# Kernel optimization log

Hardware: AMD Instinct MI355X
Metric: run time of the kernel (lower is better)

Reference implementation:

```python
import jax, jax.numpy as jnp
import numpy as np

POOL_H, POOL_W = 16, 8
NEG = -1e30
B, C = 8, 64
F_WR2 = 64 * 32 * 32          # flattened x3
D_CLS = 3 * C * POOL_H * POOL_W  # 24576, classifier input


def _adaptive_mask(starts, lens, out_size, in_size):
    """Membership mask (B, out_size, in_size) for torch-style adaptive pooling bins
    over a per-sample window [start, start+len) along an axis of length in_size."""
    i = jnp.arange(out_size)
    lo = (i[None, :] * lens[:, None]) // out_size                     # (B,O)
    hi = ((i[None, :] + 1) * lens[:, None] + out_size - 1) // out_size  # ceil
    r = jnp.arange(in_size)
    rel = r[None, None, :] - starts[:, None, None]                    # (B,1,I)
    return (rel >= lo[:, :, None]) & (rel < hi[:, :, None]) & (rel >= 0) & (rel < lens[:, None, None])


def _roi_pool(x, boxes):
    """Adaptive max pool of per-sample ROI boxes (x1,y1,x2,y2) to (16,8).
    x: (B,C,H,W,T); invalid boxes -> zeros (matches torch code's skip/zeros fallback)."""
    _, _, H, W, T = x.shape
    b = jnp.floor(boxes).astype(jnp.int32)          # torch .long() after clamp>=0
    x1, y1, x2, y2 = b[:, 0], b[:, 1], b[:, 2], b[:, 3]
    valid = (x1 >= 0) & (y1 >= 0) & (x2 < W) & (y2 < H) & (x2 > x1) & (y2 > y1)
    h = jnp.maximum(y2 - y1 + 1, 1)                 # inclusive slice y1:y2+1
    w = jnp.maximum(x2 - x1 + 1, 1)
    rowm = _adaptive_mask(y1, h, POOL_H, H)         # (B,16,H)
    colm = _adaptive_mask(x1, w, POOL_W, W)         # (B,8,W)
    # separable masked max: first over W into 8 col-bins, then over H into 16 row-bins
    s1 = jnp.max(jnp.where(colm[:, None, None, :, :, None], x[:, :, :, None, :, :], NEG), axis=4)  # (B,C,H,8,T)
    s2 = jnp.max(jnp.where(rowm[:, None, :, :, None, None], s1[:, :, None, :, :, :], NEG), axis=(3, 5))  # (B,C,16,8)
    ok = valid[:, None, None, None] & (s2 > NEG / 2)
    return jnp.where(ok, s2, 0.0)


def _forward(x1, x2, x3,
             wr2_w1, wr2_b1, wr2_w2, wr2_b2, wr2_w3, wr2_b3,
             head_w1, head_b1, w2_prov, b2_prov, w2_alpha, b2_alpha, w2_ad, b2_ad):
    bsz = x3.shape[0]
    xf = x3.reshape(bsz, -1)
    # wR2: three stacked Linears, no nonlinearity
    boxLoc = ((xf @ wr2_w1 + wr2_b1) @ wr2_w2 + wr2_b2) @ wr2_w3 + wr2_b3   # (B,4)
    postfix = jnp.array([[1., 0., 1., 0.], [0., 1., 0., 1.],
                         [-0.5, 0., 0.5, 0.], [0., -0.5, 0., 0.5]], dtype=boxLoc.dtype)
    boxNew = jnp.clip(boxLoc @ postfix, 0.0, 1.0)                           # (B,4) in [0,1]

    def scale(x):  # p matrices are diag(w,h,w,h)
        H, W = x.shape[2], x.shape[3]
        return jnp.array([W, H, W, H], dtype=boxNew.dtype)

    roi1 = _roi_pool(x1, boxNew * scale(x1))
    roi2 = _roi_pool(x2, boxNew * scale(x2))
    roi3 = _roi_pool(x3, boxNew * scale(x3))
    feat = jnp.concatenate((roi1, roi2, roi3), axis=1).reshape(bsz, -1)     # (B, 3*C*16*8)

    # 7 classifier heads: Linear(D,128) -> ReLU -> Linear(128, out_k)
    hidden = jax.nn.relu(jnp.einsum('bd,kdh->kbh', feat, head_w1) + head_b1[:, None, :])  # (7,B,128)
    o1 = hidden[0] @ w2_prov + b2_prov          # (B,38)
    o2 = hidden[1] @ w2_alpha + b2_alpha        # (B,25)
    o_ad = jnp.einsum('kbh,kho->kbo', hidden[2:], w2_ad) + b2_ad[:, None, :]  # (5,B,35)
    return (o1, o2, o_ad[0], o_ad[1], o_ad[2], o_ad[3], o_ad[4])


def setup_inputs() -> dict:
    key = jax.random.key(0)
    ks = jax.random.split(key, 16)
    inp = {
        'x1': jax.random.normal(ks[0], (B, C, 128, 128, 1), jnp.float32),
        'x2': jax.random.normal(ks[1], (B, C, 64, 64, 1), jnp.float32),
        'x3': jax.random.normal(ks[2], (B, C, 32, 32, 1), jnp.float32),
        'detection_targets': jax.random.uniform(ks[3], (B, 4), jnp.float32),
        'YI': jax.random.randint(ks[4], (B, 7), 0, 35, jnp.int32),
        # wR2 params (small weights + centered bias so predicted boxes are valid)
        'wr2_w1': jax.random.normal(ks[5], (F_WR2, 100), jnp.float32) * 1e-3,
        'wr2_b1': jnp.zeros((100,), jnp.float32),
        'wr2_w2': jax.random.normal(ks[6], (100, 100), jnp.float32) * 0.05,
        'wr2_b2': jnp.zeros((100,), jnp.float32),
        'wr2_w3': jax.random.normal(ks[7], (100, 4), jnp.float32) * 0.05,
        'wr2_b3': jnp.array([0.5, 0.5, 0.6, 0.6], jnp.float32),
        # 7 heads, first layer stacked
        'head_w1': jax.random.normal(ks[8], (7, D_CLS, 128), jnp.float32) * 0.02,
        'head_b1': jnp.zeros((7, 128), jnp.float32),
        'w2_prov': jax.random.normal(ks[9], (128, 38), jnp.float32) * 0.05,
        'b2_prov': jnp.zeros((38,), jnp.float32),
        'w2_alpha': jax.random.normal(ks[10], (128, 25), jnp.float32) * 0.05,
        'b2_alpha': jnp.zeros((25,), jnp.float32),
        'w2_ad': jax.random.normal(ks[11], (5, 128, 35), jnp.float32) * 0.05,
        'b2_ad': jnp.zeros((5, 35), jnp.float32),
    }
    return inp


def reference(x1, x2, x3, detection_targets, YI,
              wr2_w1, wr2_b1, wr2_w2, wr2_b2, wr2_w3, wr2_b3,
              head_w1, head_b1, w2_prov, b2_prov, w2_alpha, b2_alpha, w2_ad, b2_ad):
    # detection_targets / YI are accepted but unused, as in the torch forward
    del detection_targets, YI
    return _forward(x1, x2, x3, wr2_w1, wr2_b1, wr2_w2, wr2_b2, wr2_w3, wr2_b3,
                    head_w1, head_b1, w2_prov, b2_prov, w2_alpha, b2_alpha, w2_ad, b2_ad)
```

## Files before the change

### kernel.cpp

```cpp
#include <hip/hip_runtime.h>

#define Bb 8
#define Cch 64
#define D1 65536
#define D2 24576
#define NCH1 512
#define CH1 128
#define NCH2 192
#define CH2 128
#define NEGV -1e30f


__global__ __launch_bounds__(128) void k_gemm1(const float* __restrict__ x3,
                                               const float* __restrict__ w1,
                                               float* __restrict__ p1) {
    __shared__ float xs[Bb][CH1];
    int c = blockIdx.x, t = threadIdx.x;
    int d0 = c * CH1;
    #pragma unroll
    for (int b = 0; b < Bb; ++b) xs[b][t] = x3[(size_t)b * D1 + d0 + t];
    __syncthreads();
    if (t < 100) {
        float acc[Bb];
        #pragma unroll
        for (int b = 0; b < Bb; ++b) acc[b] = 0.f;
        #pragma unroll 4
        for (int dl = 0; dl < CH1; ++dl) {
            float w = w1[(size_t)(d0 + dl) * 100 + t];
            #pragma unroll
            for (int b = 0; b < Bb; ++b) acc[b] += w * xs[b][dl];
        }
        #pragma unroll
        for (int b = 0; b < Bb; ++b) p1[((size_t)c * 100 + t) * 8 + b] = acc[b];
    }
}

__global__ __launch_bounds__(64) void k_red1(const float* __restrict__ p1,
                                             const float* __restrict__ b1,
                                             float* __restrict__ h1) {
    int hb = blockIdx.x;
    int h = hb >> 3, b = hb & 7;
    int t = threadIdx.x;
    float s = 0.f;
    #pragma unroll 4
    for (int c = t; c < NCH1; c += 64) s += p1[((size_t)c * 100 + h) * 8 + b];
    for (int off = 32; off; off >>= 1) s += __shfl_down(s, off);
    if (t == 0) h1[b * 100 + h] = s + b1[h];
}

__global__ __launch_bounds__(256) void k_tail(const float* __restrict__ h1g,
                                              const float* __restrict__ w2,
                                              const float* __restrict__ b2,
                                              const float* __restrict__ w3,
                                              const float* __restrict__ b3,
                                              float* __restrict__ boxNew) {
    __shared__ float h1s[800], h2s[800], bl[32];
    int t = threadIdx.x;
    for (int i = t; i < 800; i += 256) h1s[i] = h1g[i];
    __syncthreads();
    for (int i = t; i < 800; i += 256) {
        int b = i / 100, j = i % 100;
        float s = b2[j];
        for (int k = 0; k < 100; ++k) s += h1s[b * 100 + k] * w2[k * 100 + j];
        h2s[i] = s;
    }
    __syncthreads();
    if (t < 32) {
        int b = t >> 2, m = t & 3;
        float s = b3[m];
        for (int j = 0; j < 100; ++j) s += h2s[b * 100 + j] * w3[j * 4 + m];
        bl[t] = s;
    }
    __syncthreads();
    if (t < 32) {
        int b = t >> 2, i = t & 3;
        float l0 = bl[b * 4 + 0], l1 = bl[b * 4 + 1];
        float l2 = bl[b * 4 + 2], l3 = bl[b * 4 + 3];
        float v = (i == 0) ? l0 - 0.5f * l2
                : (i == 1) ? l1 - 0.5f * l3
                : (i == 2) ? l0 + 0.5f * l2
                           : l1 + 0.5f * l3;
        boxNew[t] = fminf(fmaxf(v, 0.f), 1.f);
    }
}

__global__ __launch_bounds__(128) void k_roi(const float* __restrict__ x1,
                                             const float* __restrict__ x2,
                                             const float* __restrict__ x3,
                                             const float* __restrict__ boxNew,
                                             float* __restrict__ feat) {
    int bid = blockIdx.x;
    int s = bid >> 9, r = bid & 511;
    int b = r >> 6, c = r & 63;
    const float* x = (s == 0) ? x1 : (s == 1) ? x2 : x3;
    int H = (s == 0) ? 128 : (s == 1) ? 64 : 32;
    float bn0 = boxNew[b * 4 + 0], bn1 = boxNew[b * 4 + 1];
    float bn2 = boxNew[b * 4 + 2], bn3 = boxNew[b * 4 + 3];
    float Hf = (float)H;
    int ix1 = (int)floorf(bn0 * Hf);
    int iy1 = (int)floorf(bn1 * Hf);
    int ix2 = (int)floorf(bn2 * Hf);
    int iy2 = (int)floorf(bn3 * Hf);
    bool valid = (ix1 >= 0) && (iy1 >= 0) && (ix2 < H) && (iy2 < H) &&
                 (ix2 > ix1) && (iy2 > iy1);
    int t = threadIdx.x;
    float res = 0.f;
    if (valid) {
        int hh = iy2 - iy1 + 1, ww = ix2 - ix1 + 1;
        int ph = t >> 3, pw = t & 7;
        int rlo = (ph * hh) >> 4;
        int rhi = min((((ph + 1) * hh) + 15) >> 4, hh);
        int clo = (pw * ww) >> 3;
        int chi = min((((pw + 1) * ww) + 7) >> 3, ww);
        float m = NEGV;
        const float* base = x + (size_t)(b * Cch + c) * H * H;
        for (int rr = rlo; rr < rhi; ++rr) {
            const float* row = base + (size_t)(iy1 + rr) * H + ix1;
            for (int cc = clo; cc < chi; ++cc) m = fmaxf(m, row[cc]);
        }
        if (m > -5e29f) res = m;
    }
    feat[(size_t)b * D2 + (s * 64 + c) * 128 + t] = res;
}

__global__ __launch_bounds__(256) void k_gemm2(const float* __restrict__ feat,
                                               const float* __restrict__ hw1,
                                               float* __restrict__ p2) {
    __shared__ float fs[Bb][CH2];
    __shared__ float red[128][9];
    int bid = blockIdx.x;
    int k = bid / NCH2, c = bid % NCH2;
    int d0 = c * CH2;
    int t = threadIdx.x;
    for (int i = t; i < Bb * CH2; i += 256) {
        int b = i >> 7, dl = i & 127;
        fs[b][dl] = feat[(size_t)b * D2 + d0 + dl];
    }
    __syncthreads();
    int h = t & 127, dd = t >> 7;
    float acc[Bb];
    #pragma unroll
    for (int b = 0; b < Bb; ++b) acc[b] = 0.f;
    const float* wbase = hw1 + ((size_t)k * D2 + d0) * 128 + h;
    #pragma unroll 8
    for (int dl = dd; dl < CH2; dl += 2) {
        float w = wbase[(size_t)dl * 128];
        #pragma unroll
        for (int b = 0; b < Bb; ++b) acc[b] += w * fs[b][dl];
    }
    if (dd == 1) {
        #pragma unroll
        for (int b = 0; b < Bb; ++b) red[h][b] = acc[b];
    }
    __syncthreads();
    if (dd == 0) {
        #pragma unroll
        for (int b = 0; b < Bb; ++b) {
            float v = acc[b] + red[h][b];
            p2[(((size_t)k * NCH2 + c) * 8 + b) * 128 + h] = v;
        }
    }
}

__global__ __launch_bounds__(128) void k_out(const float* __restrict__ p2,
                                             const float* __restrict__ hb1,
                                             const float* __restrict__ w2p,
                                             const float* __restrict__ b2p,
                                             const float* __restrict__ w2a,
                                             const float* __restrict__ b2a,
                                             const float* __restrict__ w2ad,
                                             const float* __restrict__ b2ad,
                                             float* __restrict__ out) {
    __shared__ float hid[128];
    int kb = blockIdx.x;
    int k = kb >> 3, b = kb & 7;
    int t = threadIdx.x;
    float s = 0.f;
    #pragma unroll 8
    for (int c = 0; c < NCH2; ++c)
        s += p2[(((size_t)k * NCH2 + c) * 8 + b) * 128 + t];
    s += hb1[k * 128 + t];
    hid[t] = fmaxf(s, 0.f);
    __syncthreads();

    const float* w;
    const float* bias;
    int nj, off;
    if (k == 0)      { w = w2p;                    bias = b2p;               nj = 38; off = b * 38; }
    else if (k == 1) { w = w2a;                    bias = b2a;               nj = 25; off = 304 + b * 25; }
    else             { int g = k - 2;
                       w = w2ad + (size_t)g * 128 * 35; bias = b2ad + g * 35; nj = 35;
                       off = 504 + g * 280 + b * 35; }
    if (t < nj) {
        float o = bias[t];
        #pragma unroll 8
        for (int h = 0; h < 128; ++h) o += hid[h] * w[(size_t)h * nj + t];
        out[off + t] = o;
    }
}

extern "C" void kernel_launch(void* const* d_in, const int* in_sizes, int n_in,
                              void* d_out, int out_size, void* d_ws, size_t ws_size,
                              hipStream_t stream) {
    const float* x1   = (const float*)d_in[0];
    const float* x2   = (const float*)d_in[1];
    const float* x3   = (const float*)d_in[2];
    const float* w1   = (const float*)d_in[5];
    const float* b1   = (const float*)d_in[6];
    const float* w2   = (const float*)d_in[7];
    const float* b2   = (const float*)d_in[8];
    const float* w3   = (const float*)d_in[9];
    const float* b3   = (const float*)d_in[10];
    const float* hw1  = (const float*)d_in[11];
    const float* hb1  = (const float*)d_in[12];
    const float* w2p  = (const float*)d_in[13];
    const float* b2p  = (const float*)d_in[14];
    const float* w2a  = (const float*)d_in[15];
    const float* b2a  = (const float*)d_in[16];
    const float* w2ad = (const float*)d_in[17];
    const float* b2ad = (const float*)d_in[18];

    float* ws     = (float*)d_ws;
    float* boxNew = ws;
    float* h1     = ws + 32;
    float* feat   = ws + 8192;
    float* p1     = ws + 204800;
    float* p2     = ws + 614400;

    k_gemm1<<<NCH1, 128, 0, stream>>>(x3, w1, p1);
    k_red1<<<800, 64, 0, stream>>>(p1, b1, h1);
    k_tail<<<1, 256, 0, stream>>>(h1, w2, b2, w3, b3, boxNew);
    k_roi<<<1536, 128, 0, stream>>>(x1, x2, x3, boxNew, feat);
    k_gemm2<<<7 * NCH2, 256, 0, stream>>>(feat, hw1, p2);
    k_out<<<56, 128, 0, stream>>>(p2, hb1, w2p, b2p, w2a, b2a, w2ad, b2ad,
                                  (float*)d_out);
}
```

Baseline: 275.1 us.

## Split reductions across more threads in gemm1, red1, gemm2, out; stage tail weights in LDS

k_gemm1 now uses 256 threads, with two halves each covering 64 rows of the chunk and combining through shared memory. k_red1 uses one block per hidden unit that reduces all 8 batches at once, with coalesced loads. k_gemm2 has each thread load float2 weight pairs over a 4-way split of the chunk. k_out splits its chunk sum over two thread halves, and k_tail stages w2 and w3 in LDS. The aim is more memory parallelism and fewer serial dependent loads, mainly in the weight-streaming GEMMs, at the cost of extra shared-memory reductions and syncs.

Measured after the change: 259.8 us. 1.06x faster.

```diff
diff --git a/kernel.cpp b/kernel.cpp
--- a/kernel.cpp
+++ b/kernel.cpp
@@ -11,41 +11,64 @@
 #define NEGV -1e30f
 
 
-__global__ __launch_bounds__(128) void k_gemm1(const float* __restrict__ x3,
+__global__ __launch_bounds__(256) void k_gemm1(const float* __restrict__ x3,
                                                const float* __restrict__ w1,
                                                float* __restrict__ p1) {
     __shared__ float xs[Bb][CH1];
+    __shared__ float red[CH1][9];
     int c = blockIdx.x, t = threadIdx.x;
     int d0 = c * CH1;
+    for (int i = t; i < Bb * CH1; i += 256) {
+        int b = i >> 7, r = i & 127;
+        xs[b][r] = x3[(size_t)b * D1 + d0 + r];
+    }
+    __syncthreads();
+    int j = t & 127, sub = t >> 7;
+    float acc[Bb];
     #pragma unroll
-    for (int b = 0; b < Bb; ++b) xs[b][t] = x3[(size_t)b * D1 + d0 + t];
-    __syncthreads();
-    if (t < 100) {
-        float acc[Bb];
-        #pragma unroll
-        for (int b = 0; b < Bb; ++b) acc[b] = 0.f;
-        #pragma unroll 4
-        for (int dl = 0; dl < CH1; ++dl) {
-            float w = w1[(size_t)(d0 + dl) * 100 + t];
+    for (int b = 0; b < Bb; ++b) acc[b] = 0.f;
+    if (j < 100) {
+        const float* wb = w1 + (size_t)(d0 + sub * 64) * 100 + j;
+        #pragma unroll 8
+        for (int r0 = 0; r0 < 64; ++r0) {
+            float w = wb[(size_t)r0 * 100];
+            int r = sub * 64 + r0;
             #pragma unroll
-            for (int b = 0; b < Bb; ++b) acc[b] += w * xs[b][dl];
-        }
-        #pragma unroll
-        for (int b = 0; b < Bb; ++b) p1[((size_t)c * 100 + t) * 8 + b] = acc[b];
-    }
-}
-
-__global__ __launch_bounds__(64) void k_red1(const float* __restrict__ p1,
-                                             const float* __restrict__ b1,
-                                             float* __restrict__ h1) {
-    int hb = blockIdx.x;
-    int h = hb >> 3, b = hb & 7;
-    int t = threadIdx.x;
+            for (int b = 0; b < Bb; ++b) acc[b] += w * xs[b][r];
+        }
+    }
+    if (sub == 1 && j < 100) {
+        #pragma unroll
+        for (int b = 0; b < Bb; ++b) red[j][b] = acc[b];
+    }
+    __syncthreads();
+    if (sub == 0 && j < 100) {
+        #pragma unroll
+        for (int b = 0; b < Bb; ++b)
+            p1[((size_t)c * 100 + j) * 8 + b] = acc[b] + red[j][b];
+    }
+}
+
+__global__ __launch_bounds__(256) void k_red1(const float* __restrict__ p1,
+                                              const float* __restrict__ b1,
+                                              float* __restrict__ h1) {
+    __shared__ float red[4][8];
+    int h = blockIdx.x;
+    int t = threadIdx.x;
+    int b = t & 7, c0 = t >> 3;
     float s = 0.f;
-    #pragma unroll 4
-    for (int c = t; c < NCH1; c += 64) s += p1[((size_t)c * 100 + h) * 8 + b];
-    for (int off = 32; off; off >>= 1) s += __shfl_down(s, off);
-    if (t == 0) h1[b * 100 + h] = s + b1[h];
+    #pragma unroll
+    for (int i = 0; i < 16; ++i) {
+        int c = c0 + 32 * i;
+        s += p1[((size_t)c * 100 + h) * 8 + b];
+    }
+    for (int off = 32; off >= 8; off >>= 1) s += __shfl_down(s, off);
+    if ((t & 63) < 8) red[t >> 6][t & 7] = s;
+    __syncthreads();
+    if (t < 8) {
+        float v = red[0][t] + red[1][t] + red[2][t] + red[3][t] + b1[h];
+        h1[t * 100 + h] = v;
+    }
 }
 
 __global__ __launch_bounds__(256) void k_tail(const float* __restrict__ h1g,
@@ -55,20 +78,26 @@
                                               const float* __restrict__ b3,
                                               float* __restrict__ boxNew) {
     __shared__ float h1s[800], h2s[800], bl[32];
-    int t = threadIdx.x;
+    __shared__ float w2s[10000];
+    __shared__ float w3s[400];
+    int t = threadIdx.x;
+    for (int i = t; i < 10000; i += 256) w2s[i] = w2[i];
     for (int i = t; i < 800; i += 256) h1s[i] = h1g[i];
+    for (int i = t; i < 400; i += 256) w3s[i] = w3[i];
     __syncthreads();
     for (int i = t; i < 800; i += 256) {
         int b = i / 100, j = i % 100;
         float s = b2[j];
-        for (int k = 0; k < 100; ++k) s += h1s[b * 100 + k] * w2[k * 100 + j];
+        #pragma unroll 4
+        for (int k = 0; k < 100; ++k) s += h1s[b * 100 + k] * w2s[k * 100 + j];
         h2s[i] = s;
     }
     __syncthreads();
     if (t < 32) {
         int b = t >> 2, m = t & 3;
         float s = b3[m];
-        for (int j = 0; j < 100; ++j) s += h2s[b * 100 + j] * w3[j * 4 + m];
+        #pragma unroll 4
+        for (int j = 0; j < 100; ++j) s += h2s[b * 100 + j] * w3s[j * 4 + m];
         bl[t] = s;
     }
     __syncthreads();
@@ -127,7 +156,7 @@
                                                const float* __restrict__ hw1,
                                                float* __restrict__ p2) {
     __shared__ float fs[Bb][CH2];
-    __shared__ float red[128][9];
+    __shared__ float red[3][64][17];
     int bid = blockIdx.x;
     int k = bid / NCH2, c = bid % NCH2;
     int d0 = c * CH2;
@@ -137,32 +166,43 @@
         fs[b][dl] = feat[(size_t)b * D2 + d0 + dl];
     }
     __syncthreads();
-    int h = t & 127, dd = t >> 7;
-    float acc[Bb];
+    int l = t & 63, sub = t >> 6;
+    int h2 = l * 2;
+    float accx[Bb], accy[Bb];
     #pragma unroll
-    for (int b = 0; b < Bb; ++b) acc[b] = 0.f;
-    const float* wbase = hw1 + ((size_t)k * D2 + d0) * 128 + h;
+    for (int b = 0; b < Bb; ++b) { accx[b] = 0.f; accy[b] = 0.f; }
+    const float* wbase = hw1 + ((size_t)k * D2 + d0) * 128 + h2;
     #pragma unroll 8
-    for (int dl = dd; dl < CH2; dl += 2) {
-        float w = wbase[(size_t)dl * 128];
-        #pragma unroll
-        for (int b = 0; b < Bb; ++b) acc[b] += w * fs[b][dl];
-    }
-    if (dd == 1) {
-        #pragma unroll
-        for (int b = 0; b < Bb; ++b) red[h][b] = acc[b];
-    }
-    __syncthreads();
-    if (dd == 0) {
+    for (int i = 0; i < 32; ++i) {
+        int dl = sub + 4 * i;
+        float2 w = *(const float2*)&wbase[(size_t)dl * 128];
         #pragma unroll
         for (int b = 0; b < Bb; ++b) {
-            float v = acc[b] + red[h][b];
-            p2[(((size_t)k * NCH2 + c) * 8 + b) * 128 + h] = v;
-        }
-    }
-}
-
-__global__ __launch_bounds__(128) void k_out(const float* __restrict__ p2,
+            float f = fs[b][dl];
+            accx[b] += w.x * f;
+            accy[b] += w.y * f;
+        }
+    }
+    if (sub) {
+        #pragma unroll
+        for (int b = 0; b < Bb; ++b) {
+            red[sub - 1][l][b * 2]     = accx[b];
+            red[sub - 1][l][b * 2 + 1] = accy[b];
+        }
+    }
+    __syncthreads();
+    if (sub == 0) {
+        #pragma unroll
+        for (int b = 0; b < Bb; ++b) {
+            float vx = accx[b] + red[0][l][b * 2]     + red[1][l][b * 2]     + red[2][l][b * 2];
+            float vy = accy[b] + red[0][l][b * 2 + 1] + red[1][l][b * 2 + 1] + red[2][l][b * 2 + 1];
+            float2 v = make_float2(vx, vy);
+            *(float2*)&p2[(((size_t)k * NCH2 + c) * 8 + b) * 128 + h2] = v;
+        }
+    }
+}
+
+__global__ __launch_bounds__(256) void k_out(const float* __restrict__ p2,
                                              const float* __restrict__ hb1,
                                              const float* __restrict__ w2p,
                                              const float* __restrict__ b2p,
@@ -172,15 +212,18 @@
                                              const float* __restrict__ b2ad,
                                              float* __restrict__ out) {
     __shared__ float hid[128];
+    __shared__ float red[128];
     int kb = blockIdx.x;
     int k = kb >> 3, b = kb & 7;
     int t = threadIdx.x;
+    int h = t & 127, sub = t >> 7;
     float s = 0.f;
     #pragma unroll 8
-    for (int c = 0; c < NCH2; ++c)
-        s += p2[(((size_t)k * NCH2 + c) * 8 + b) * 128 + t];
-    s += hb1[k * 128 + t];
-    hid[t] = fmaxf(s, 0.f);
+    for (int c = sub; c < NCH2; c += 2)
+        s += p2[(((size_t)k * NCH2 + c) * 8 + b) * 128 + h];
+    if (sub) red[h] = s;
+    __syncthreads();
+    if (!sub) hid[h] = fmaxf(s + red[h] + hb1[k * 128 + h], 0.f);
     __syncthreads();
 
     const float* w;
@@ -194,7 +237,7 @@
     if (t < nj) {
         float o = bias[t];
         #pragma unroll 8
-        for (int h = 0; h < 128; ++h) o += hid[h] * w[(size_t)h * nj + t];
+        for (int hh = 0; hh < 128; ++hh) o += hid[hh] * w[(size_t)hh * nj + t];
         out[off + t] = o;
     }
 }
@@ -227,11 +270,11 @@
     float* p1     = ws + 204800;
     float* p2     = ws + 614400;
 
-    k_gemm1<<<NCH1, 128, 0, stream>>>(x3, w1, p1);
-    k_red1<<<800, 64, 0, stream>>>(p1, b1, h1);
+    k_gemm1<<<NCH1, 256, 0, stream>>>(x3, w1, p1);
+    k_red1<<<100, 256, 0, stream>>>(p1, b1, h1);
     k_tail<<<1, 256, 0, stream>>>(h1, w2, b2, w3, b3, boxNew);
     k_roi<<<1536, 128, 0, stream>>>(x1, x2, x3, boxNew, feat);
     k_gemm2<<<7 * NCH2, 256, 0, stream>>>(feat, hw1, p2);
-    k_out<<<56, 128, 0, stream>>>(p2, hb1, w2p, b2p, w2a, b2a, w2ad, b2ad,
+    k_out<<<56, 256, 0, stream>>>(p2, hb1, w2p, b2p, w2a, b2a, w2ad, b2ad,
                                   (float*)d_out);
 }
```
